# Kernel optimization log

Measured on AMD Instinct MI355X. Metric: run time of the kernel, lower is better.

## Reference

```python
import jax, jax.numpy as jnp
import numpy as np
from jax import lax

# SLAYER neuron / simulation constants (netParams)
THETA = 1.0      # spike threshold
TAU_SR = 4.0     # PSP (SRM) kernel time constant
TAU_REF = 1.0    # refractory kernel time constant
SCALE_REF = 2.0  # refractory scale (kernel amplitude = -scaleRef*theta)
TAU_RHO = 1.0    # surrogate-gradient width (used in bwd only)
SCALE_RHO = 1.0

B, F_IN, T = 8, 6300, 500  # 6300 = 50*63*2
HID, OUT = 32, 20


def _alpha_scan(x, d):
    """Causal conv with alpha kernel k*d**k along last (time) axis via 2-state recurrence.
    x: [..., T]. y[t] = sum_{j<=t} x[j]*(t-j)*d**(t-j)."""
    xt = jnp.moveaxis(x, -1, 0)  # [T, ...]
    zero = jnp.zeros_like(xt[0])

    def step(carry, xi):
        z, y = carry
        y_new = d * (y + z)       # y[t] = d*(y[t-1] + z[t-1])
        z_new = d * z + xi        # z[t] = d*z[t-1] + x[t]
        return (z_new, y_new), y_new

    _, ys = lax.scan(step, (zero, zero), xt)
    return jnp.moveaxis(ys, 0, -1)


def psp(x):
    """SLAYER psp: convolve spike train with SRM kernel eps(k) = (k/tauSr)*exp(1-k/tauSr)."""
    d = float(np.exp(-1.0 / TAU_SR))
    return jnp.float32(np.e / TAU_SR) * _alpha_scan(x, d)


def _spike_impl(p):
    """Iterative threshold + refractory. p: [..., T] membrane input (post-psp, post-dense).
    Refractory kernel: ref(k) = -scaleRef*theta*(k/tauRef)*exp(1-k/tauRef), realized by the
    same 2-state alpha recurrence driven by emitted spikes."""
    d = float(np.exp(-1.0 / TAU_REF))
    C = jnp.float32(-SCALE_REF * THETA * np.e / TAU_REF)
    pt = jnp.moveaxis(p, -1, 0)  # [T, ...]
    zero = jnp.zeros_like(pt[0])

    def step(carry, pi):
        z, y = carry
        y_new = d * (y + z)                 # alpha state from past spikes (lag>=1)
        u = pi + C * y_new                  # membrane potential incl. refractory
        s = (u >= THETA).astype(pi.dtype)   # hard threshold
        z_new = d * z + s
        return (z_new, y_new), s

    _, ss = lax.scan(step, (zero, zero), pt)
    return jnp.moveaxis(ss, 0, -1)


def spike(p):
    return _spike_impl(p)


def setup_inputs() -> dict:
    key = jax.random.key(0)
    k1, k2, k3 = jax.random.split(key, 3)
    downsampled = (jax.random.uniform(k1, (B, F_IN, T)) < 0.05).astype(jnp.float32)
    w1 = jax.random.normal(k2, (HID, F_IN), jnp.float32) * 0.05
    w2 = jax.random.normal(k3, (OUT, HID), jnp.float32) * 0.3
    return {"downsampled": downsampled, "w1": w1, "w2": w2}


def reference(downsampled, w1, w2):
    # spike_1 = spike(psp(downsampled))
    s1 = spike(psp(downsampled))
    # spike_2 = spike(fc1(psp(spike_1)))
    s2 = spike(jnp.einsum('of,bft->bot', w1, psp(s1)))
    # spike_3 = spike(fc2(psp(spike_2)))
    s3 = spike(jnp.einsum('of,bft->bot', w2, psp(s2)))
    return s3
```

## Files before the change

### kernel.cpp

```cpp
#include <hip/hip_runtime.h>
#include <stdint.h>

#define NB 8
#define F_IN 6300
#define NT 500
#define HID 32
#define NOUT 20
#define NW 99

#define D_SR   0.7788007830714049f
#define S_SR   0.6795704571147613f
#define D_REF  0.36787944117144233f
#define C_REF  -5.43656365691809f

__global__ __launch_bounds__(256) void k0_transpose(const float* __restrict__ w1,
                                                    float* __restrict__ w1t) {
  __shared__ float tl[64][33];
  const int f0 = blockIdx.x * 64;
  const int tid = threadIdx.x;
  const int r = tid & 63, g = tid >> 6;
#pragma unroll
  for (int oo = 0; oo < 32; oo += 4) {
    int o = oo + g;
    int f = f0 + r;
    tl[r][o] = (f < F_IN) ? w1[o * F_IN + f] : 0.f;
  }
  __syncthreads();
#pragma unroll
  for (int k = 0; k < 8; k++) {
    int idx = k * 256 + tid;
    int rr = idx >> 5, cc = idx & 31;
    int f = f0 + rr;
    if (f < F_IN) w1t[(size_t)f * 32 + cc] = tl[rr][cc];
  }
}

#define CH_T 100

__global__ __launch_bounds__(64) void k1_layer1(const float* __restrict__ x,
                                                uint64_t* __restrict__ masks) {
  __shared__ float tile[CH_T][65];
  const int wi = blockIdx.x;
  const int b  = blockIdx.y;
  const int lane = threadIdx.x;
  const int f = wi * 64 + lane;
  const float vm = (f < F_IN) ? 1.0f : 0.0f;
  const float* xblk = x + (size_t)b * F_IN * NT;
  uint64_t* mrow = masks + ((size_t)b * NW + wi) * NT;

  int goff[25], fidv[25], jv[25];
#pragma unroll
  for (int k = 0; k < 25; k++) {
    int idx = k * 64 + lane;
    int fid = idx / 25;
    int j = idx - fid * 25;
    int rf = wi * 64 + fid;
    if (rf >= F_IN) rf = F_IN - 1;
    goff[k] = rf * NT + 4 * j;
    fidv[k] = fid;
    jv[k] = j;
  }

  float z1 = 0.f, y1 = 0.f, zr = 0.f, yr = 0.f;
  float4 ld[25];
#pragma unroll
  for (int k = 0; k < 25; k++) ld[k] = *(const float4*)(xblk + goff[k]);

  for (int c = 0; c < 5; c++) {
#pragma unroll
    for (int k = 0; k < 25; k++) {
      int r = 4 * jv[k], fd = fidv[k];
      tile[r + 0][fd] = ld[k].x;
      tile[r + 1][fd] = ld[k].y;
      tile[r + 2][fd] = ld[k].z;
      tile[r + 3][fd] = ld[k].w;
    }
    if (c + 1 < 5) {
      const float* gb = xblk + (c + 1) * CH_T;
#pragma unroll
      for (int k = 0; k < 25; k++) ld[k] = *(const float4*)(gb + goff[k]);
    }
    uint64_t keep0 = 0, keep1 = 0;
#pragma unroll
    for (int tc = 0; tc < CH_T; tc++) {
      float xi = tile[tc][lane] * vm;
      y1 = __fmul_rn(D_SR, __fadd_rn(y1, z1));
      z1 = __fadd_rn(__fmul_rn(D_SR, z1), xi);
      float p = __fmul_rn(S_SR, y1);
      yr = __fmul_rn(D_REF, __fadd_rn(yr, zr));
      float u = __fadd_rn(p, __fmul_rn(C_REF, yr));
      bool s = (u >= 1.0f);
      zr = __fadd_rn(__fmul_rn(D_REF, zr), s ? 1.0f : 0.0f);
      uint64_t m = __ballot(s);
      if (tc < 64) { if (lane == tc)      keep0 = m; }
      else         { if (lane == tc - 64) keep1 = m; }
    }
    uint64_t* mp = mrow + c * CH_T;
    mp[lane] = keep0;
    if (lane < CH_T - 64) mp[64 + lane] = keep1;
  }
}

__global__ __launch_bounds__(512) void k2_fc1(const float* __restrict__ w1t,
                                              const uint64_t* __restrict__ masks,
                                              double* __restrict__ R) {
  __shared__ double part[8][32];
  const int tid = threadIdx.x;
  const int wv = tid >> 6;
  const int lane = tid & 63;
  const int half = lane >> 5;
  const int o = lane & 31;
  const int b = blockIdx.x;
  const int t = blockIdx.y * 4 + (wv & 3);
  const int seg = wv >> 2;
  const int wbeg = seg * 50, wend = seg ? NW : 50;
  const uint64_t* mbase = masks + (size_t)b * NW * NT + t;
  const char* wrow = (const char*)w1t + o * 4;
  double acc = 0.0;

  int wi = wbeg + half;
  uint64_t mcur = (wi < wend) ? mbase[(size_t)wi * NT] : 0;
  for (; wi < wend; wi += 2) {
    uint64_t mnext = (wi + 2 < wend) ? mbase[(size_t)(wi + 2) * NT] : 0;
    const uint32_t base0 = ((uint32_t)wi << 13);
    uint32_t w = (uint32_t)mcur;
    uint32_t boff = base0;
#pragma unroll
    for (int sub = 0; sub < 2; sub++) {
      while (w) {
        uint32_t i0 = __builtin_ctz(w);                 uint32_t w1_ = w & (w - 1);
        uint32_t i1 = w1_ ? __builtin_ctz(w1_) : 0u;    uint32_t w2_ = w1_ ? (w1_ & (w1_ - 1)) : 0u;
        uint32_t i2 = w2_ ? __builtin_ctz(w2_) : 0u;    uint32_t w3_ = w2_ ? (w2_ & (w2_ - 1)) : 0u;
        uint32_t i3 = w3_ ? __builtin_ctz(w3_) : 0u;    w = w3_ ? (w3_ & (w3_ - 1)) : 0u;
        float a0 = *(const float*)(wrow + boff + (i0 << 7));
        float a1 = *(const float*)(wrow + boff + (i1 << 7));
        float a2 = *(const float*)(wrow + boff + (i2 << 7));
        float a3 = *(const float*)(wrow + boff + (i3 << 7));
        a1 = w1_ ? a1 : 0.0f;
        a2 = w2_ ? a2 : 0.0f;
        a3 = w3_ ? a3 : 0.0f;
        acc += (double)a0;
        acc += (double)a1;
        acc += (double)a2;
        acc += (double)a3;
      }
      w = (uint32_t)(mcur >> 32);
      boff = base0 + (32u << 7);
    }
    mcur = mnext;
  }
  int hi2 = __shfl_xor(__double2hiint(acc), 32);
  int lo2 = __shfl_xor(__double2loint(acc), 32);
  acc += __hiloint2double(hi2, lo2);
  if (half == 0) part[wv][o] = acc;
  __syncthreads();
  if (wv < 4 && half == 0) {
    double tot = part[wv][o] + part[wv + 4][o];
    R[((size_t)b * HID + o) * NT + t] = tot;
  }
}

__device__ __forceinline__ bool snn_step(double ri, double& z2, double& y2,
                                         double& zr, double& yr) {
  const double dsr = (double)D_SR, ssr = (double)S_SR;
  const double dre = (double)D_REF, cr = (double)C_REF;
  y2 = dsr * (y2 + z2);
  z2 = dsr * z2 + ri;
  double p = ssr * y2;
  yr = dre * (yr + zr);
  double u = p + cr * yr;
  bool s = (u >= 1.0);
  zr = dre * zr + (s ? 1.0 : 0.0);
  return s;
}

__global__ __launch_bounds__(256) void k345(const double* __restrict__ R,
                                            const float* __restrict__ w2,
                                            float* __restrict__ out) {
  __shared__ uint32_t s2m[NT];
  __shared__ float    w2l[NOUT][33];
  __shared__ double   r3[NT][NOUT];
  const int tid = threadIdx.x;
  const int b = blockIdx.x;

  if (tid >= 64) {
    for (int i = tid - 64; i < NOUT * HID; i += 192)
      w2l[i >> 5][i & 31] = w2[i];
  } else {
    const int lane = tid;
    const int h = lane & 31;
    const bool act = lane < HID;
    const double2* r2 = (const double2*)(R + ((size_t)b * HID + h) * NT);
    double z2 = 0, y2 = 0, zr = 0, yr = 0;
    double2 g0a = r2[0], g0b = r2[1];
    double2 g1a = r2[2], g1b = r2[3];
    double2 g2a = r2[4], g2b = r2[5];
    double2 g3a = r2[6], g3b = r2[7];
    for (int g = 0; g < 125; g++) {
      const int t = g * 4;
      double v0 = act ? g0a.x : 0.0, v1 = act ? g0a.y : 0.0;
      double v2 = act ? g0b.x : 0.0, v3 = act ? g0b.y : 0.0;
      uint64_t m0 = __ballot(snn_step(v0, z2, y2, zr, yr) && act);
      uint64_t m1 = __ballot(snn_step(v1, z2, y2, zr, yr) && act);
      uint64_t m2 = __ballot(snn_step(v2, z2, y2, zr, yr) && act);
      uint64_t m3 = __ballot(snn_step(v3, z2, y2, zr, yr) && act);
      if (lane == 0) {
        s2m[t + 0] = (uint32_t)m0;
        s2m[t + 1] = (uint32_t)m1;
        s2m[t + 2] = (uint32_t)m2;
        s2m[t + 3] = (uint32_t)m3;
      }
      g0a = g1a; g0b = g1b; g1a = g2a; g1b = g2b; g2a = g3a; g2b = g3b;
      if (g + 4 < 125) { g3a = r2[(g + 4) * 2]; g3b = r2[(g + 4) * 2 + 1]; }
    }
  }
  __syncthreads();

  if (tid < 240) {
    const int o = tid / 12;
    const int sl = tid % 12;
    for (int t = sl; t < NT; t += 12) {
      uint32_t m = s2m[t];
      double acc = 0.0;
      while (m) {
        int i = __builtin_ctz(m);
        m &= m - 1;
        acc += (double)w2l[o][i];
      }
      r3[t][o] = acc;
    }
  }
  __syncthreads();

  if (tid < NOUT) {
    const int o = tid;
    float* orow = out + ((size_t)b * NOUT + o) * NT;
    double z2 = 0, y2 = 0, zr = 0, yr = 0;
    for (int t = 0; t < NT; t++) {
      bool s = snn_step(r3[t][o], z2, y2, zr, yr);
      orow[t] = s ? 1.0f : 0.0f;
    }
  }
}

extern "C" void kernel_launch(void* const* d_in, const int* in_sizes, int n_in,
                              void* d_out, int out_size, void* d_ws, size_t ws_size,
                              hipStream_t stream) {
  const float* x  = (const float*)d_in[0];
  const float* w1 = (const float*)d_in[1];
  const float* w2 = (const float*)d_in[2];
  float* out = (float*)d_out;

  uint8_t* ws = (uint8_t*)d_ws;
  const size_t W1T_BYTES  = (size_t)F_IN * HID * 4;
  const size_t MASK_BYTES = (size_t)NB * NW * NT * 8;
  float*    w1t   = (float*)ws;
  uint64_t* masks = (uint64_t*)(ws + W1T_BYTES);
  double*   R     = (double*)(ws + W1T_BYTES + MASK_BYTES);

  k0_transpose<<<99, 256, 0, stream>>>(w1, w1t);
  k1_layer1<<<dim3(NW, NB), 64, 0, stream>>>(x, masks);
  k2_fc1<<<dim3(NB, NT / 4), 512, 0, stream>>>(w1t, masks, R);
  k345<<<NB, 256, 0, stream>>>(R, w2, out);
}
```

Before: 316.2 us.

## Split layer-2/3 kernel into three kernels with shortened spike recurrence

Replaces the single per-batch k345 kernel, which ran its stages serially inside one block, with three kernels. A spike-2 kernel packs two batches per wavefront so no lanes sit idle. A fully parallel fc2 kernel gives one thread per (b,o,t), and a final spike kernel uses one thread per output row. The spike recurrence is algebraically restructured with FMAs, and the dependence on the current spike moves to a select on the previous spike, shortening the serial critical path. The cost is two extra kernel launches and global round trips for s2m and R3, and the FMA reassociation may change threshold decisions slightly in double precision.

Result: slower. 350.8 us (+11.0%).

```diff
diff --git a/kernel.cpp b/kernel.cpp
--- a/kernel.cpp
+++ b/kernel.cpp
@@ -160,86 +160,118 @@
   }
 }
 
-__device__ __forceinline__ bool snn_step(double ri, double& z2, double& y2,
-                                         double& zr, double& yr) {
+#define SNN_FAST_STEP(rin, EMIT)                                                \
+  {                                                                             \
+    y2 = __builtin_fma(dsr, y2, w);                                   \
+    z2 = __builtin_fma(dsr, z2, (rin));                               \
+    w  = dsr * z2;                                                              \
+    double p  = ssr * y2;                                                       \
+    double u0 = __builtin_fma(cr, q, p);                                        \
+    double u1 = u0 + K;                                                         \
+    double u  = sp ? u1 : u0;                                                   \
+    bool s = (u >= 1.0);                                                        \
+    double yr = q + (sp ? dre : 0.0);                                 \
+    double zr = zrd + (sp ? 1.0 : 0.0);                           \
+    zrd = dre * zr;                                                             \
+    q = __builtin_fma(dre, yr, dre * zrd);                             \
+    sp = s;                                                                     \
+    EMIT                                                                        \
+  }
+
+__global__ __launch_bounds__(64) void k3_spike2(const double* __restrict__ R,
+                                                uint32_t* __restrict__ s2m) {
+  const int blk = blockIdx.x;
+  const int lane = threadIdx.x;
+  const int half = lane >> 5;
+  const int b = blk * 2 + half;
+  const int h = lane & 31;
+  const double2* r2 = (const double2*)(R + ((size_t)b * HID + h) * NT);
+  uint32_t* m0 = s2m + (size_t)(blk * 2) * NT;
+  uint32_t* m1 = s2m + (size_t)(blk * 2 + 1) * NT;
+
   const double dsr = (double)D_SR, ssr = (double)S_SR;
   const double dre = (double)D_REF, cr = (double)C_REF;
-  y2 = dsr * (y2 + z2);
-  z2 = dsr * z2 + ri;
-  double p = ssr * y2;
-  yr = dre * (yr + zr);
-  double u = p + cr * yr;
-  bool s = (u >= 1.0);
-  zr = dre * zr + (s ? 1.0 : 0.0);
-  return s;
-}
-
-__global__ __launch_bounds__(256) void k345(const double* __restrict__ R,
-                                            const float* __restrict__ w2,
-                                            float* __restrict__ out) {
-  __shared__ uint32_t s2m[NT];
-  __shared__ float    w2l[NOUT][33];
-  __shared__ double   r3[NT][NOUT];
+  const double K = cr * dre;
+  double y2 = 0, z2 = 0, w = 0, q = 0, zrd = 0;
+  bool sp = false;
+
+  double2 g0a = r2[0], g0b = r2[1];
+  double2 g1a = r2[2], g1b = r2[3];
+  double2 g2a = r2[4], g2b = r2[5];
+  double2 g3a = r2[6], g3b = r2[7];
+  for (int g = 0; g < 125; g++) {
+    const int t = g * 4;
+    SNN_FAST_STEP(g0a.x, { uint64_t m = __ballot(s);
+      if (lane == 0) { m0[t] = (uint32_t)m; m1[t] = (uint32_t)(m >> 32); } })
+    SNN_FAST_STEP(g0a.y, { uint64_t m = __ballot(s);
+      if (lane == 0) { m0[t + 1] = (uint32_t)m; m1[t + 1] = (uint32_t)(m >> 32); } })
+    SNN_FAST_STEP(g0b.x, { uint64_t m = __ballot(s);
+      if (lane == 0) { m0[t + 2] = (uint32_t)m; m1[t + 2] = (uint32_t)(m >> 32); } })
+    SNN_FAST_STEP(g0b.y, { uint64_t m = __ballot(s);
+      if (lane == 0) { m0[t + 3] = (uint32_t)m; m1[t + 3] = (uint32_t)(m >> 32); } })
+    g0a = g1a; g0b = g1b; g1a = g2a; g1b = g2b; g2a = g3a; g2b = g3b;
+    if (g + 4 < 125) { g3a = r2[(g + 4) * 2]; g3b = r2[(g + 4) * 2 + 1]; }
+  }
+}
+
+__global__ __launch_bounds__(256) void k4_fc2(const float* __restrict__ w2,
+                                              const uint32_t* __restrict__ s2m,
+                                              double* __restrict__ R3) {
+  __shared__ float w2l[NOUT * HID];
   const int tid = threadIdx.x;
-  const int b = blockIdx.x;
-
-  if (tid >= 64) {
-    for (int i = tid - 64; i < NOUT * HID; i += 192)
-      w2l[i >> 5][i & 31] = w2[i];
-  } else {
-    const int lane = tid;
-    const int h = lane & 31;
-    const bool act = lane < HID;
-    const double2* r2 = (const double2*)(R + ((size_t)b * HID + h) * NT);
-    double z2 = 0, y2 = 0, zr = 0, yr = 0;
-    double2 g0a = r2[0], g0b = r2[1];
-    double2 g1a = r2[2], g1b = r2[3];
-    double2 g2a = r2[4], g2b = r2[5];
-    double2 g3a = r2[6], g3b = r2[7];
-    for (int g = 0; g < 125; g++) {
-      const int t = g * 4;
-      double v0 = act ? g0a.x : 0.0, v1 = act ? g0a.y : 0.0;
-      double v2 = act ? g0b.x : 0.0, v3 = act ? g0b.y : 0.0;
-      uint64_t m0 = __ballot(snn_step(v0, z2, y2, zr, yr) && act);
-      uint64_t m1 = __ballot(snn_step(v1, z2, y2, zr, yr) && act);
-      uint64_t m2 = __ballot(snn_step(v2, z2, y2, zr, yr) && act);
-      uint64_t m3 = __ballot(snn_step(v3, z2, y2, zr, yr) && act);
-      if (lane == 0) {
-        s2m[t + 0] = (uint32_t)m0;
-        s2m[t + 1] = (uint32_t)m1;
-        s2m[t + 2] = (uint32_t)m2;
-        s2m[t + 3] = (uint32_t)m3;
-      }
-      g0a = g1a; g0b = g1b; g1a = g2a; g1b = g2b; g2a = g3a; g2b = g3b;
-      if (g + 4 < 125) { g3a = r2[(g + 4) * 2]; g3b = r2[(g + 4) * 2 + 1]; }
-    }
-  }
+  for (int i = tid; i < NOUT * HID; i += 256) w2l[i] = w2[i];
   __syncthreads();
-
-  if (tid < 240) {
-    const int o = tid / 12;
-    const int sl = tid % 12;
-    for (int t = sl; t < NT; t += 12) {
-      uint32_t m = s2m[t];
-      double acc = 0.0;
-      while (m) {
-        int i = __builtin_ctz(m);
-        m &= m - 1;
-        acc += (double)w2l[o][i];
-      }
-      r3[t][o] = acc;
-    }
-  }
-  __syncthreads();
-
-  if (tid < NOUT) {
-    const int o = tid;
-    float* orow = out + ((size_t)b * NOUT + o) * NT;
-    double z2 = 0, y2 = 0, zr = 0, yr = 0;
-    for (int t = 0; t < NT; t++) {
-      bool s = snn_step(r3[t][o], z2, y2, zr, yr);
-      orow[t] = s ? 1.0f : 0.0f;
-    }
+  int id = blockIdx.x * 256 + tid;
+  if (id >= NB * NOUT * NT) return;
+  int t = id % NT;
+  int bo = id / NT;
+  int o = bo % NOUT;
+  int b = bo / NOUT;
+  uint32_t m = s2m[(size_t)b * NT + t];
+  const float* wr = w2l + o * HID;
+  double acc = 0.0;
+  while (m) {
+    uint32_t i0 = __builtin_ctz(m);                 uint32_t m1_ = m & (m - 1);
+    uint32_t i1 = m1_ ? __builtin_ctz(m1_) : 0u;    uint32_t m2_ = m1_ ? (m1_ & (m1_ - 1)) : 0u;
+    uint32_t i2 = m2_ ? __builtin_ctz(m2_) : 0u;    uint32_t m3_ = m2_ ? (m2_ & (m2_ - 1)) : 0u;
+    uint32_t i3 = m3_ ? __builtin_ctz(m3_) : 0u;    m = m3_ ? (m3_ & (m3_ - 1)) : 0u;
+    float a0 = wr[i0];
+    float a1 = m1_ ? wr[i1] : 0.0f;
+    float a2 = m2_ ? wr[i2] : 0.0f;
+    float a3 = m3_ ? wr[i3] : 0.0f;
+    acc += (double)a0;
+    acc += (double)a1;
+    acc += (double)a2;
+    acc += (double)a3;
+  }
+  R3[id] = acc;
+}
+
+__global__ __launch_bounds__(64) void k5_out(const double* __restrict__ R3,
+                                             float* __restrict__ out) {
+  int id = blockIdx.x * 64 + threadIdx.x;
+  if (id >= NB * NOUT) return;
+  const double2* r2 = (const double2*)(R3 + (size_t)id * NT);
+  float* orow = out + (size_t)id * NT;
+
+  const double dsr = (double)D_SR, ssr = (double)S_SR;
+  const double dre = (double)D_REF, cr = (double)C_REF;
+  const double K = cr * dre;
+  double y2 = 0, z2 = 0, w = 0, q = 0, zrd = 0;
+  bool sp = false;
+
+  double2 g0a = r2[0], g0b = r2[1];
+  double2 g1a = r2[2], g1b = r2[3];
+  double2 g2a = r2[4], g2b = r2[5];
+  double2 g3a = r2[6], g3b = r2[7];
+  for (int g = 0; g < 125; g++) {
+    SNN_FAST_STEP(g0a.x, { orow[0] = s ? 1.0f : 0.0f; })
+    SNN_FAST_STEP(g0a.y, { orow[1] = s ? 1.0f : 0.0f; })
+    SNN_FAST_STEP(g0b.x, { orow[2] = s ? 1.0f : 0.0f; })
+    SNN_FAST_STEP(g0b.y, { orow[3] = s ? 1.0f : 0.0f; })
+    orow += 4;
+    g0a = g1a; g0b = g1b; g1a = g2a; g1b = g2b; g2a = g3a; g2b = g3b;
+    if (g + 4 < 125) { g3a = r2[(g + 4) * 2]; g3b = r2[(g + 4) * 2 + 1]; }
   }
 }
 
@@ -254,12 +286,18 @@
   uint8_t* ws = (uint8_t*)d_ws;
   const size_t W1T_BYTES  = (size_t)F_IN * HID * 4;
   const size_t MASK_BYTES = (size_t)NB * NW * NT * 8;
+  const size_t R_BYTES    = (size_t)NB * HID * NT * 8;
+  const size_t S2M_BYTES  = (size_t)NB * NT * 4;
   float*    w1t   = (float*)ws;
   uint64_t* masks = (uint64_t*)(ws + W1T_BYTES);
   double*   R     = (double*)(ws + W1T_BYTES + MASK_BYTES);
+  uint32_t* s2m   = (uint32_t*)(ws + W1T_BYTES + MASK_BYTES + R_BYTES);
+  double*   R3    = (double*)(ws + W1T_BYTES + MASK_BYTES + R_BYTES + S2M_BYTES);
 
   k0_transpose<<<99, 256, 0, stream>>>(w1, w1t);
   k1_layer1<<<dim3(NW, NB), 64, 0, stream>>>(x, masks);
   k2_fc1<<<dim3(NB, NT / 4), 512, 0, stream>>>(w1t, masks, R);
-  k345<<<NB, 256, 0, stream>>>(R, w2, out);
-}
+  k3_spike2<<<4, 64, 0, stream>>>(R, s2m);
+  k4_fc2<<<(NB * NOUT * NT + 255) / 256, 256, 0, stream>>>(w2, s2m, R3);
+  k5_out<<<3, 64, 0, stream>>>(R3, out);
+}
```
